# Kernel optimization log

Measured on AMD Instinct MI355X. Metric: run time of the kernel, lower is better.

Reference implementation:

```python
import math
import jax, jax.numpy as jnp
import numpy as np

B, NV, C = 8, 512, 256
H, R = 6, 32
PAIR_H = 16
RBF_K = 8


def setup_inputs() -> dict:
    key = jax.random.key(0)
    ks = jax.random.split(key, 12)
    s = lambda fan_in: 1.0 / math.sqrt(fan_in)
    inp = {
        'feats': jax.random.normal(ks[0], (B, 2 * NV + 1, C), jnp.float32),
        'xy': jax.random.uniform(ks[1], (B, NV, 2), jnp.float32),
        'Wq': jax.random.normal(ks[2], (C, H * R), jnp.float32) * s(C),
        'Wk': jax.random.normal(ks[3], (C, H * R), jnp.float32) * s(C),
        'Wpi': jax.random.normal(ks[4], (C, PAIR_H), jnp.float32) * s(C),
        'bpi': jnp.zeros((PAIR_H,), jnp.float32),
        'Wpj': jax.random.normal(ks[5], (C, PAIR_H), jnp.float32) * s(C),
        'bpj': jnp.zeros((PAIR_H,), jnp.float32),
        'gW1': jax.random.normal(ks[6], (2 + RBF_K + 2, 32), jnp.float32) * s(12),
        'gb1': jnp.zeros((32,), jnp.float32),
        'gW2': jax.random.normal(ks[7], (32, 1), jnp.float32) * s(32),
        'gb2': jnp.zeros((1,), jnp.float32),
        'aW1': jax.random.normal(ks[8], (6, 16), jnp.float32) * s(6),
        'ab1': jnp.zeros((16,), jnp.float32),
        'aW2': jax.random.normal(ks[9], (16, 1), jnp.float32) * s(16),
        'ab2': jnp.zeros((1,), jnp.float32),
        'dW': jax.random.normal(ks[10], (C, 1), jnp.float32) * s(C),
        'db': jnp.zeros((1,), jnp.float32),
        'alpha_pair': jnp.float32(0.5),
        'alpha_geom': jnp.float32(0.6),
        'alpha_angle': jnp.float32(0.6),
        'logit_scale': jnp.float32(1.0),
    }
    return inp


def _pos_scale(p, lo=0.0, hi=1.5):
    return lo + (hi - lo) * jax.nn.sigmoid(p)


def _logit_scale_fn(p, lo=0.5, hi=3.0):
    return lo + (hi - lo) * jax.nn.sigmoid(p)


def reference(feats, xy, Wq, Wk, Wpi, bpi, Wpj, bpj, gW1, gb1, gW2, gb2,
              aW1, ab1, aW2, ab2, dW, db,
              alpha_pair, alpha_geom, alpha_angle, logit_scale):
    # fold vertices: drop BOS, average (y, x) token pairs -> [B, N, C]
    x = feats[:, 1:]
    Bb, L, Cc = x.shape
    x = x.reshape(Bb, L // 2, 2, Cc).mean(axis=2)
    N = x.shape[1]

    # multi-head low-rank bilinear core, summed over heads
    Q = (x @ Wq).reshape(Bb, N, H, R)
    K = (x @ Wk).reshape(Bb, N, H, R)
    S = jnp.einsum('bnhr,bmhr->bnm', Q, K) / math.sqrt(R)

    # separable pair nonlinearity (outer product of tiny ReLU features)
    a_i = jax.nn.relu(x @ Wpi + bpi)
    b_j = jax.nn.relu(x @ Wpj + bpj)
    S = S + _pos_scale(alpha_pair) * jnp.einsum('bnd,bmd->bnm', a_i, b_j)

    # geometry / angle biases
    yv, xv = xy[..., 0], xy[..., 1]
    dy = yv[:, :, None] - yv[:, None, :]          # [B,N,N]
    dx = xv[:, :, None] - xv[:, None, :]
    theta = jnp.arctan2(dy, dx)
    pad_i = (jnp.abs(yv) < 1e-9) & (jnp.abs(xv) < 1e-9)
    pad_pair = pad_i[:, :, None] | pad_i[:, None, :]
    c1, s1 = jnp.cos(theta), jnp.sin(theta)

    # distance RBF + cos/sin bias
    rbf_mu = jnp.linspace(0.0, math.sqrt(2.0), RBF_K).astype(jnp.float32)
    spacing = rbf_mu[1] - rbf_mu[0]
    rbf_gamma = 1.0 / (2.0 * spacing ** 2 + 1e-8)
    r = jnp.sqrt(dy * dy + dx * dx + 1e-8)
    phi = jnp.exp(-rbf_gamma * (r[..., None] - rbf_mu) ** 2)  # [B,N,N,K]
    geom_feat = jnp.concatenate(
        [dy[..., None], dx[..., None], phi, c1[..., None], s1[..., None]], axis=-1)
    G = (jax.nn.relu(geom_feat @ gW1 + gb1) @ gW2 + gb2)[..., 0]
    G = jnp.where(pad_pair, 0.0, G)
    S = S + _pos_scale(alpha_geom) * G

    # angle harmonics (theta, 2theta, 4theta)
    c2, s2 = jnp.cos(2.0 * theta), jnp.sin(2.0 * theta)
    c4, s4 = jnp.cos(4.0 * theta), jnp.sin(4.0 * theta)
    ang_feat = jnp.stack([c1, s1, c2, s2, c4, s4], axis=-1)  # [B,N,N,6]
    Hb = (jax.nn.relu(ang_feat @ aW1 + ab1) @ aW2 + ab2)[..., 0]
    Hb = jnp.where(pad_pair, 0.0, Hb)
    S = S + _pos_scale(alpha_angle) * Hb

    # diagonal bias and bounded global scale
    d = (x @ dW + db)[..., 0]                     # [B,N]
    idx = jnp.arange(N)
    S = S.at[:, idx, idx].add(d)
    S = S * _logit_scale_fn(logit_scale)
    return S
```

## Files before the change

### kernel.cpp

```cpp
#include <hip/hip_runtime.h>
#include <math.h>


#define UK 224

typedef __attribute__((ext_vector_type(8)))  short short8;
typedef __attribute__((ext_vector_type(16))) float f32x16;
typedef __attribute__((ext_vector_type(4)))  int   int4v;

__device__ __forceinline__ float sigmoidf_(float x){ return 1.0f/(1.0f + __expf(-x)); }
__device__ __forceinline__ unsigned f2bf(float x){
    unsigned u = __builtin_bit_cast(unsigned, x);
    return (u + 0x7fffu + ((u>>16)&1u)) >> 16;
}
__device__ __forceinline__ unsigned pk2(float lo, float hi){
    unsigned r;
    asm("v_cvt_pk_bf16_f32 %0, %1, %2" : "=v"(r) : "v"(lo), "v"(hi));
    return r;
}
__device__ __forceinline__ f32x16 zero16(){
    f32x16 z;
    #pragma unroll
    for (int i = 0; i < 16; i++) z[i] = 0.f;
    return z;
}

__global__ __launch_bounds__(256) void k_prep(const float* __restrict__ feats,
        const float* __restrict__ Wq, const float* __restrict__ Wk,
        const float* __restrict__ Wpi, const float* __restrict__ bpi,
        const float* __restrict__ Wpj, const float* __restrict__ bpj,
        const float* __restrict__ dW, const float* __restrict__ db,
        const float* __restrict__ a_pair,
        unsigned short* __restrict__ xb, unsigned short* __restrict__ WT,
        float* __restrict__ bcat){
    int blk = blockIdx.x, tid = threadIdx.x;
    if (blk < 4096){
        int b = blk >> 9, n = blk & 511;
        size_t base = ((size_t)(b*1025 + 1 + 2*n))*256 + tid;
        float v = 0.5f*(feats[base] + feats[base+256]);
        xb[(size_t)blk*256 + tid] = (unsigned short)f2bf(v);
    } else {
        int col = blk - 4096;
        int c   = tid;
        const float invSqrtR = 0.17677669529663687f;
        float sp = 1.5f*sigmoidf_(a_pair[0]);
        float v;
        if      (col < 192)  v = Wq[c*192 + col]*invSqrtR;
        else if (col < 208)  v = sp*Wpi[c*16 + (col-192)];
        else if (col < 400)  v = Wk[c*192 + (col-208)];
        else if (col < 416)  v = Wpj[c*16 + (col-400)];
        else if (col == 416) v = dW[c];
        else v = 0.f;
        WT[col*256 + c] = (unsigned short)f2bf(v);
        if (tid == 0){
            float bv = 0.f;
            if      (col >= 192 && col < 208) bv = sp*bpi[col-192];
            else if (col >= 400 && col < 416) bv = bpj[col-400];
            else if (col == 416)              bv = db[0];
            bcat[col] = bv;
        }
    }
}

__global__ __launch_bounds__(256) void k_uv(const unsigned short* __restrict__ xb,
        const unsigned short* __restrict__ WT, const float* __restrict__ bcat,
        unsigned short* __restrict__ Ub, unsigned short* __restrict__ Vb,
        float* __restrict__ dv){
    int tid = threadIdx.x;
    int lane = tid & 63, l31 = lane & 31, hf = lane >> 5;
    int w = tid >> 6, wr = w >> 1, wc = w & 1;
    int c0 = blockIdx.x*64, r0 = blockIdx.y*64;
    const unsigned short* ap = xb + (size_t)(r0 + wr*32 + l31)*256 + 8*hf;
    const unsigned short* bp = WT + (size_t)(c0 + wc*32 + l31)*256 + 8*hf;
    f32x16 acc = zero16();
    #pragma unroll 4
    for (int k0 = 0; k0 < 256; k0 += 16){
        short8 a  = *(const short8*)(ap + k0);
        short8 bb = *(const short8*)(bp + k0);
        acc = __builtin_amdgcn_mfma_f32_32x32x16_bf16(a, bb, acc, 0, 0, 0);
    }
    int col = c0 + wc*32 + l31;
    int rb  = r0 + wr*32 + 4*hf;
    float bc = bcat[col];
    #pragma unroll
    for (int r = 0; r < 16; r++){
        int row = rb + (r&3) + 8*(r>>2);
        float v = acc[r] + bc;
        size_t ui = (size_t)row*UK;
        if (col < 208){
            if (col >= 192) v = fmaxf(v, 0.f);
            Ub[ui + col] = (unsigned short)f2bf(v);
        } else if (col < 224){
            Vb[ui + col-208] = (unsigned short)f2bf(v);
            Ub[ui + col] = 0;
        } else if (col < 416){
            if (col >= 400) v = fmaxf(v, 0.f);
            Vb[ui + col-208] = (unsigned short)f2bf(v);
        } else if (col == 416){
            dv[row] = v;
            Vb[ui + 208] = 0;
        } else if (col < 432){
            Vb[ui + col-208] = 0;
        }
    }
}

__global__ __launch_bounds__(256) void k_gemm(const unsigned short* __restrict__ Ub,
        const unsigned short* __restrict__ Vb, float* __restrict__ S){
    int tid = threadIdx.x;
    int lane = tid & 63, l31 = lane & 31, hf = lane >> 5;
    int w = tid >> 6, wr = w >> 1, wc = w & 1;
    int b = blockIdx.z;
    int m0 = blockIdx.x*64, n0 = blockIdx.y*64;
    const unsigned short* ap = Ub + (size_t)(b*512 + n0 + wr*32 + l31)*UK + 8*hf;
    const unsigned short* bp = Vb + (size_t)(b*512 + m0 + wc*32 + l31)*UK + 8*hf;
    f32x16 acc = zero16();
    #pragma unroll 2
    for (int k0 = 0; k0 < UK; k0 += 16){
        short8 a  = *(const short8*)(ap + k0);
        short8 bb = *(const short8*)(bp + k0);
        acc = __builtin_amdgcn_mfma_f32_32x32x16_bf16(a, bb, acc, 0, 0, 0);
    }
    int m  = m0 + wc*32 + l31;
    int nb = n0 + wr*32 + 4*hf;
    float* Sp = S + ((size_t)b*512)*512 + m;
    #pragma unroll
    for (int r = 0; r < 16; r++){
        int n = nb + (r&3) + 8*(r>>2);
        Sp[(size_t)n*512] = acc[r];
    }
}

__global__ __launch_bounds__(256, 3) void k_pairs(const float* __restrict__ xy,
        const float* __restrict__ gW1, const float* __restrict__ gb1,
        const float* __restrict__ gW2, const float* __restrict__ gb2,
        const float* __restrict__ aW1, const float* __restrict__ ab1,
        const float* __restrict__ aW2, const float* __restrict__ ab2,
        const float* __restrict__ dv,
        const float* __restrict__ a_geom, const float* __restrict__ a_ang,
        const float* __restrict__ lsc,
        float* __restrict__ S){
    int tid  = threadIdx.x;
    int lane = tid & 63;
    int hf   = lane >> 5;
    int l31  = lane & 31;

    float sg = 1.5f*sigmoidf_(a_geom[0]);
    float sa = 1.5f*sigmoidf_(a_ang[0]);
    float ls = 0.5f + 2.5f*sigmoidf_(lsc[0]);

    short8 wg, wa;
    #pragma unroll
    for (int j = 0; j < 8; j++){
        int f = hf*8 + j;
        float vg = (f < 12) ? gW1[f*32 + l31] : 0.f;
        float va = (f >= 10 && l31 < 16) ? aW1[(f-10)*16 + l31] : 0.f;
        wg[j] = (short)f2bf(vg);
        wa[j] = (short)f2bf(va);
    }

    float nbg[16], g2g[16], nba[16], g2a[16];
    float bsum = 0.f;
    #pragma unroll
    for (int r = 0; r < 16; r++){
        int h = (r&3) + 8*(r>>2) + 4*hf;
        float bg  = gb1[h];
        float wg2 = sg*gW2[h];
        nbg[r] = -bg; g2g[r] = wg2; bsum += bg*wg2;
        if (h < 16){
            float ba  = ab1[h];
            float wa2 = sa*aW2[h];
            nba[r] = -ba; g2a[r] = wa2; bsum += ba*wa2;
        } else { nba[r] = 0.f; g2a[r] = 0.f; }
    }
    bsum += __shfl_xor(bsum, 32);
    float cb = sg*gb2[0] + sa*ab2[0] + bsum;

    const float GAMMA = 12.2499985f;
    const float TWOGD = 4.9497469f;

    int wid = __builtin_amdgcn_readfirstlane(tid >> 6);
    int wave_g = blockIdx.x*4 + wid;
    for (int c = wave_g; c < 32768; c += 3072){
        int base = c*64;
        int nn = (base >> 9) & 511;
        int bb = base >> 18;
        const float* xyb = xy + (size_t)bb*1024;
        float yn = xyb[2*nn], xn = xyb[2*nn+1];
        bool padn = (fabsf(yn) < 1e-9f) && (fabsf(xn) < 1e-9f);
        float sv  = S[(size_t)base + lane];
        float dvn = dv[bb*512 + nn];

        unsigned fA0, fA1, fA2, fA3, fB0, fB1, fB2, fB3;
        float mA, mB;
        #pragma unroll
        for (int ch = 0; ch < 2; ch++){
            int pidx = base + ch*32 + l31;
            float2 pm = *(const float2*)(xyb + 2*(pidx & 511));
            float ym = pm.x, xm = pm.y;
            bool padm = (fabsf(ym) < 1e-9f) && (fabsf(xm) < 1e-9f);
            float msk = (padn || padm) ? 0.f : 1.f;
            float dy = yn - ym, dx = xn - xm;
            float r2 = dy*dy + dx*dx;
            float re = sqrtf(r2 + 1e-8f);
            float c1, s1;
            if (r2 > 0.f){ float inv = rsqrtf(r2); c1 = dx*inv; s1 = dy*inv; }
            else { c1 = 1.f; s1 = 0.f; }
            float c2 = c1*c1 - s1*s1, s2 = 2.f*c1*s1;
            float c4 = c2*c2 - s2*s2, s4 = 2.f*c2*s2;
            float e0 = __expf(-GAMMA*(r2 + 1e-8f));
            float E  = __expf(TWOGD*re);
            float u  = e0;
            float p0 = u;
            u *= E; float p1 = 0.60653066f*u;
            u *= E; float p2 = 0.13533528f*u;
            u *= E; float p3 = 0.011108997f*u;
            u *= E; float p4 = 3.3546263e-4f*u;
            u *= E; float p5 = 3.7266532e-6f*u;
            u *= E; float p6 = 1.5229979e-8f*u;
            u *= E; float p7 = 2.2897348e-11f*u;
            unsigned w0 = hf ? pk2(p6, p7) : pk2(dy, dx);
            unsigned w1 = hf ? pk2(c1, s1) : pk2(p0, p1);
            unsigned w2 = hf ? pk2(c2, s2) : pk2(p2, p3);
            unsigned w3 = hf ? pk2(c4, s4) : pk2(p4, p5);
            if (ch == 0){ fA0=w0; fA1=w1; fA2=w2; fA3=w3; mA = msk; }
            else        { fB0=w0; fB1=w1; fB2=w2; fB3=w3; mB = msk; }
        }
        int4v ivA = {(int)fA0, (int)fA1, (int)fA2, (int)fA3};
        int4v ivB = {(int)fB0, (int)fB1, (int)fB2, (int)fB3};
        short8 bfA = __builtin_bit_cast(short8, ivA);
        short8 bfB = __builtin_bit_cast(short8, ivB);

        f32x16 z = zero16();
        f32x16 dgA = __builtin_amdgcn_mfma_f32_32x32x16_bf16(wg, bfA, z, 0, 0, 0);
        f32x16 dgB = __builtin_amdgcn_mfma_f32_32x32x16_bf16(wg, bfB, z, 0, 0, 0);
        f32x16 daA = __builtin_amdgcn_mfma_f32_32x32x16_bf16(wa, bfA, z, 0, 0, 0);
        f32x16 daB = __builtin_amdgcn_mfma_f32_32x32x16_bf16(wa, bfB, z, 0, 0, 0);

        float accA = 0.f, accB = 0.f;
        #pragma unroll
        for (int r = 0; r < 16; r++){
            accA += fmaxf(dgA[r], nbg[r]) * g2g[r];
            accB += fmaxf(dgB[r], nbg[r]) * g2g[r];
        }
        #pragma unroll
        for (int r = 0; r < 16; r++){
            accA += fmaxf(daA[r], nba[r]) * g2a[r];
            accB += fmaxf(daB[r], nba[r]) * g2a[r];
        }
        accA += __shfl_xor(accA, 32);
        accB += __shfl_xor(accB, 32);

        float res  = (lane < 32) ? accA : accB;
        float mskw = (lane < 32) ? mA : mB;
        int m_w = (base + lane) & 511;
        float ddg = (m_w == nn) ? dvn : 0.f;
        S[(size_t)base + lane] = (sv + mskw*(res + cb) + ddg) * ls;
    }
}

extern "C" void kernel_launch(void* const* d_in, const int* in_sizes, int n_in,
                              void* d_out, int out_size, void* d_ws, size_t ws_size,
                              hipStream_t stream){
    const float* feats = (const float*)d_in[0];
    const float* xy    = (const float*)d_in[1];
    const float* Wq    = (const float*)d_in[2];
    const float* Wk    = (const float*)d_in[3];
    const float* Wpi   = (const float*)d_in[4];
    const float* bpi   = (const float*)d_in[5];
    const float* Wpj   = (const float*)d_in[6];
    const float* bpj   = (const float*)d_in[7];
    const float* gW1   = (const float*)d_in[8];
    const float* gb1   = (const float*)d_in[9];
    const float* gW2   = (const float*)d_in[10];
    const float* gb2   = (const float*)d_in[11];
    const float* aW1   = (const float*)d_in[12];
    const float* ab1   = (const float*)d_in[13];
    const float* aW2   = (const float*)d_in[14];
    const float* ab2   = (const float*)d_in[15];
    const float* dW    = (const float*)d_in[16];
    const float* db    = (const float*)d_in[17];
    const float* a_pair= (const float*)d_in[18];
    const float* a_geom= (const float*)d_in[19];
    const float* a_ang = (const float*)d_in[20];
    const float* lsc   = (const float*)d_in[21];

    float* S = (float*)d_out;
    char* wsb = (char*)d_ws;
    unsigned short* xb = (unsigned short*)wsb;
    unsigned short* WT = (unsigned short*)(wsb + 2097152);
    unsigned short* Ub = (unsigned short*)(wsb + 2326528);
    unsigned short* Vb = (unsigned short*)(wsb + 4161536);
    float* bcat = (float*)(wsb + 5996544);
    float* dv   = (float*)(wsb + 5998336);

    k_prep <<<4544, 256, 0, stream>>>(feats, Wq, Wk, Wpi, bpi, Wpj, bpj, dW, db, a_pair,
                                      xb, WT, bcat);
    k_uv   <<<dim3(7,64), 256, 0, stream>>>(xb, WT, bcat, Ub, Vb, dv);
    k_gemm <<<dim3(8,8,8), 256, 0, stream>>>(Ub, Vb, S);
    k_pairs<<<768, 256, 0, stream>>>(xy, gW1, gb1, gW2, gb2, aW1, ab1, aW2, ab2,
                                     dv, a_geom, a_ang, lsc, S);
}
```

Measured before the change: 57.16 us.

## Compute pair features once per lane and exchange halves via shuffles

Previously each lane computed features for two pair columns, once per 32-lane half, so the transcendental and RBF work was duplicated. Now each lane computes the features for its own pair column once, and packed bf16 fragments are exchanged across the two 32-lane halves with shuffles to build the MFMA B operands. The epilogue weights are split into uniform per-half copies made scalar with readfirstlane, and the per-lane weight arrays are replaced by a branch on the half index. The grid grows from 768 to 1024 blocks. The cost is four extra cross-lane shuffles per chunk plus divergent-looking (though wave-uniform per half) epilogue code and higher register pressure.

After: 55.38 us. 3.1% less time.

```diff
diff --git a/kernel.cpp b/kernel.cpp
--- a/kernel.cpp
+++ b/kernel.cpp
@@ -17,6 +17,9 @@
     unsigned r;
     asm("v_cvt_pk_bf16_f32 %0, %1, %2" : "=v"(r) : "v"(lo), "v"(hi));
     return r;
+}
+__device__ __forceinline__ float rfl(float x){
+    return __builtin_bit_cast(float, __builtin_amdgcn_readfirstlane(__builtin_bit_cast(int, x)));
 }
 __device__ __forceinline__ f32x16 zero16(){
     f32x16 z;
@@ -145,9 +148,9 @@
     int hf   = lane >> 5;
     int l31  = lane & 31;
 
-    float sg = 1.5f*sigmoidf_(a_geom[0]);
-    float sa = 1.5f*sigmoidf_(a_ang[0]);
-    float ls = 0.5f + 2.5f*sigmoidf_(lsc[0]);
+    float sg = rfl(1.5f*sigmoidf_(a_geom[0]));
+    float sa = rfl(1.5f*sigmoidf_(a_ang[0]));
+    float ls = rfl(0.5f + 2.5f*sigmoidf_(lsc[0]));
 
     short8 wg, wa;
     #pragma unroll
@@ -159,19 +162,27 @@
         wa[j] = (short)f2bf(va);
     }
 
-    float nbg[16], g2g[16], nba[16], g2a[16];
+    float nbg0[16], g2g0[16], nbg1[16], g2g1[16];
+    float nba0[16], g2a0[16], nba1[16], g2a1[16];
     float bsum = 0.f;
     #pragma unroll
     for (int r = 0; r < 16; r++){
-        int h = (r&3) + 8*(r>>2) + 4*hf;
-        float bg  = gb1[h];
-        float wg2 = sg*gW2[h];
-        nbg[r] = -bg; g2g[r] = wg2; bsum += bg*wg2;
-        if (h < 16){
-            float ba  = ab1[h];
-            float wa2 = sa*aW2[h];
-            nba[r] = -ba; g2a[r] = wa2; bsum += ba*wa2;
-        } else { nba[r] = 0.f; g2a[r] = 0.f; }
+        int h0 = (r&3) + 8*(r>>2);
+        int h1 = h0 + 4;
+        nbg0[r] = rfl(-gb1[h0]);  g2g0[r] = rfl(sg*gW2[h0]);
+        nbg1[r] = rfl(-gb1[h1]);  g2g1[r] = rfl(sg*gW2[h1]);
+        float bg  = hf ? -nbg1[r] : -nbg0[r];
+        float wg2 = hf ?  g2g1[r] :  g2g0[r];
+        bsum += bg*wg2;
+        if (h0 < 16){
+            nba0[r] = rfl(-ab1[h0]);  g2a0[r] = rfl(sa*aW2[h0]);
+        } else { nba0[r] = 0.f; g2a0[r] = 0.f; }
+        if (h1 < 16){
+            nba1[r] = rfl(-ab1[h1]);  g2a1[r] = rfl(sa*aW2[h1]);
+        } else { nba1[r] = 0.f; g2a1[r] = 0.f; }
+        float ba  = hf ? -nba1[r] : -nba0[r];
+        float wa2 = hf ?  g2a1[r] :  g2a0[r];
+        bsum += ba*wa2;
     }
     bsum += __shfl_xor(bsum, 32);
     float cb = sg*gb2[0] + sa*ab2[0] + bsum;
@@ -181,7 +192,7 @@
 
     int wid = __builtin_amdgcn_readfirstlane(tid >> 6);
     int wave_g = blockIdx.x*4 + wid;
-    for (int c = wave_g; c < 32768; c += 3072){
+    for (int c = wave_g; c < 32768; c += 4096){
         int base = c*64;
         int nn = (base >> 9) & 511;
         int bb = base >> 18;
@@ -190,44 +201,46 @@
         bool padn = (fabsf(yn) < 1e-9f) && (fabsf(xn) < 1e-9f);
         float sv  = S[(size_t)base + lane];
         float dvn = dv[bb*512 + nn];
-
-        unsigned fA0, fA1, fA2, fA3, fB0, fB1, fB2, fB3;
-        float mA, mB;
-        #pragma unroll
-        for (int ch = 0; ch < 2; ch++){
-            int pidx = base + ch*32 + l31;
-            float2 pm = *(const float2*)(xyb + 2*(pidx & 511));
-            float ym = pm.x, xm = pm.y;
-            bool padm = (fabsf(ym) < 1e-9f) && (fabsf(xm) < 1e-9f);
-            float msk = (padn || padm) ? 0.f : 1.f;
-            float dy = yn - ym, dx = xn - xm;
-            float r2 = dy*dy + dx*dx;
-            float re = sqrtf(r2 + 1e-8f);
-            float c1, s1;
-            if (r2 > 0.f){ float inv = rsqrtf(r2); c1 = dx*inv; s1 = dy*inv; }
-            else { c1 = 1.f; s1 = 0.f; }
-            float c2 = c1*c1 - s1*s1, s2 = 2.f*c1*s1;
-            float c4 = c2*c2 - s2*s2, s4 = 2.f*c2*s2;
-            float e0 = __expf(-GAMMA*(r2 + 1e-8f));
-            float E  = __expf(TWOGD*re);
-            float u  = e0;
-            float p0 = u;
-            u *= E; float p1 = 0.60653066f*u;
-            u *= E; float p2 = 0.13533528f*u;
-            u *= E; float p3 = 0.011108997f*u;
-            u *= E; float p4 = 3.3546263e-4f*u;
-            u *= E; float p5 = 3.7266532e-6f*u;
-            u *= E; float p6 = 1.5229979e-8f*u;
-            u *= E; float p7 = 2.2897348e-11f*u;
-            unsigned w0 = hf ? pk2(p6, p7) : pk2(dy, dx);
-            unsigned w1 = hf ? pk2(c1, s1) : pk2(p0, p1);
-            unsigned w2 = hf ? pk2(c2, s2) : pk2(p2, p3);
-            unsigned w3 = hf ? pk2(c4, s4) : pk2(p4, p5);
-            if (ch == 0){ fA0=w0; fA1=w1; fA2=w2; fA3=w3; mA = msk; }
-            else        { fB0=w0; fB1=w1; fB2=w2; fB3=w3; mB = msk; }
-        }
-        int4v ivA = {(int)fA0, (int)fA1, (int)fA2, (int)fA3};
-        int4v ivB = {(int)fB0, (int)fB1, (int)fB2, (int)fB3};
+        int m_w = (base + lane) & 511;
+        float ddg = (m_w == nn) ? dvn : 0.f;
+
+        float2 pm = *(const float2*)(xyb + 2*m_w);
+        float ym = pm.x, xm = pm.y;
+        bool padm = (fabsf(ym) < 1e-9f) && (fabsf(xm) < 1e-9f);
+        float msk = (padn || padm) ? 0.f : 1.f;
+        float dy = yn - ym, dx = xn - xm;
+        float r2 = dy*dy + dx*dx;
+        float re = sqrtf(r2 + 1e-8f);
+        float c1, s1;
+        if (r2 > 0.f){ float inv = rsqrtf(r2); c1 = dx*inv; s1 = dy*inv; }
+        else { c1 = 1.f; s1 = 0.f; }
+        float c2 = c1*c1 - s1*s1, s2 = 2.f*c1*s1;
+        float c4 = c2*c2 - s2*s2, s4 = 2.f*c2*s2;
+        float e0 = __expf(-GAMMA*(r2 + 1e-8f));
+        float E  = __expf(TWOGD*re);
+        float u  = e0;
+        float p0 = u;
+        u *= E; float p1 = 0.60653066f*u;
+        u *= E; float p2 = 0.13533528f*u;
+        u *= E; float p3 = 0.011108997f*u;
+        u *= E; float p4 = 3.3546263e-4f*u;
+        u *= E; float p5 = 3.7266532e-6f*u;
+        u *= E; float p6 = 1.5229979e-8f*u;
+        u *= E; float p7 = 2.2897348e-11f*u;
+        unsigned pk0 = pk2(dy, dx), pk1 = pk2(p0, p1), pk2_ = pk2(p2, p3), pk3 = pk2(p4, p5);
+        unsigned pk4 = pk2(p6, p7), pk5 = pk2(c1, s1), pk6 = pk2(c2, s2), pk7 = pk2(c4, s4);
+
+        int s0 = __shfl_xor((int)(hf ? pk0 : pk4), 32);
+        int s1i= __shfl_xor((int)(hf ? pk1 : pk5), 32);
+        int s2i= __shfl_xor((int)(hf ? pk2_: pk6), 32);
+        int s3i= __shfl_xor((int)(hf ? pk3 : pk7), 32);
+
+        int fA0 = hf ? s0 : (int)pk0, fA1 = hf ? s1i : (int)pk1;
+        int fA2 = hf ? s2i : (int)pk2_, fA3 = hf ? s3i : (int)pk3;
+        int fB0 = hf ? (int)pk4 : s0,  fB1 = hf ? (int)pk5 : s1i;
+        int fB2 = hf ? (int)pk6 : s2i, fB3 = hf ? (int)pk7 : s3i;
+        int4v ivA = {fA0, fA1, fA2, fA3};
+        int4v ivB = {fB0, fB1, fB2, fB3};
         short8 bfA = __builtin_bit_cast(short8, ivA);
         short8 bfB = __builtin_bit_cast(short8, ivB);
 
@@ -238,24 +251,28 @@
         f32x16 daB = __builtin_amdgcn_mfma_f32_32x32x16_bf16(wa, bfB, z, 0, 0, 0);
 
         float accA = 0.f, accB = 0.f;
-        #pragma unroll
-        for (int r = 0; r < 16; r++){
-            accA += fmaxf(dgA[r], nbg[r]) * g2g[r];
-            accB += fmaxf(dgB[r], nbg[r]) * g2g[r];
-        }
-        #pragma unroll
-        for (int r = 0; r < 16; r++){
-            accA += fmaxf(daA[r], nba[r]) * g2a[r];
-            accB += fmaxf(daB[r], nba[r]) * g2a[r];
+        if (hf == 0){
+            #pragma unroll
+            for (int r = 0; r < 16; r++){
+                accA += fmaxf(dgA[r], nbg0[r]) * g2g0[r];
+                accB += fmaxf(dgB[r], nbg0[r]) * g2g0[r];
+                accA += fmaxf(daA[r], nba0[r]) * g2a0[r];
+                accB += fmaxf(daB[r], nba0[r]) * g2a0[r];
+            }
+        } else {
+            #pragma unroll
+            for (int r = 0; r < 16; r++){
+                accA += fmaxf(dgA[r], nbg1[r]) * g2g1[r];
+                accB += fmaxf(dgB[r], nbg1[r]) * g2g1[r];
+                accA += fmaxf(daA[r], nba1[r]) * g2a1[r];
+                accB += fmaxf(daB[r], nba1[r]) * g2a1[r];
+            }
         }
         accA += __shfl_xor(accA, 32);
         accB += __shfl_xor(accB, 32);
 
-        float res  = (lane < 32) ? accA : accB;
-        float mskw = (lane < 32) ? mA : mB;
-        int m_w = (base + lane) & 511;
-        float ddg = (m_w == nn) ? dvn : 0.f;
-        S[(size_t)base + lane] = (sv + mskw*(res + cb) + ddg) * ls;
+        float res = (lane < 32) ? accA : accB;
+        S[(size_t)base + lane] = (sv + msk*(res + cb) + ddg) * ls;
     }
 }
 
@@ -298,6 +315,6 @@
                                       xb, WT, bcat);
     k_uv   <<<dim3(7,64), 256, 0, stream>>>(xb, WT, bcat, Ub, Vb, dv);
     k_gemm <<<dim3(8,8,8), 256, 0, stream>>>(Ub, Vb, S);
-    k_pairs<<<768, 256, 0, stream>>>(xy, gW1, gb1, gW2, gb2, aW1, ab1, aW2, ab2,
-                                     dv, a_geom, a_ang, lsc, S);
-}
+    k_pairs<<<1024, 256, 0, stream>>>(xy, gW1, gb1, gW2, gb2, aW1, ab1, aW2, ab2,
+                                      dv, a_geom, a_ang, lsc, S);
+}
```
